# Optimization experiments

Hardware: AMD Instinct MI355X
Metric: run time of the kernel (lower is better)

The kernel has to match this reference:

```python
import jax, jax.numpy as jnp
import numpy as np

EMBED = 64
HEADS = 4
HEAD_DIM = EMBED // HEADS
N, T = 1024, 36


def setup_inputs() -> dict:
    key = jax.random.key(0)
    ks = jax.random.split(key, 8)
    scale = 1.0 / np.sqrt(HEAD_DIM)
    return {
        "values": jax.random.normal(ks[0], (N, T, EMBED), dtype=jnp.float32),
        "keys": jax.random.normal(ks[1], (N, T, EMBED), dtype=jnp.float32),
        "query": jax.random.normal(ks[2], (N, T, EMBED), dtype=jnp.float32),
        "Wv": jax.random.normal(ks[3], (HEAD_DIM, HEAD_DIM), dtype=jnp.float32) * scale,
        "Wk": jax.random.normal(ks[4], (HEAD_DIM, HEAD_DIM), dtype=jnp.float32) * scale,
        "Wq": jax.random.normal(ks[5], (HEAD_DIM, HEAD_DIM), dtype=jnp.float32) * scale,
        "Wo": jax.random.normal(ks[6], (EMBED, EMBED), dtype=jnp.float32) * (1.0 / np.sqrt(EMBED)),
        "bo": jax.random.normal(ks[7], (EMBED,), dtype=jnp.float32) * 0.01,
    }


def reference(values, keys, query, Wv, Wk, Wq, Wo, bo):
    n, t, c = query.shape
    h, d = HEADS, HEAD_DIM
    v = values.reshape(n, t, h, d)
    k = keys.reshape(n, t, h, d)
    q = query.reshape(n, t, h, d)
    # nn.Linear(head_dim, head_dim, bias=False): x @ W.T
    v = jnp.einsum('nthd,ed->nthe', v, Wv)
    k = jnp.einsum('nthd,ed->nthe', k, Wk)
    q = jnp.einsum('nthd,ed->nthe', q, Wq)
    # attention over the node dim: energy [N_q, N_k, T, H]
    energy = jnp.einsum('qthd,kthd->qkth', q, k)
    attention = jax.nn.softmax(energy / jnp.sqrt(jnp.float32(c)), axis=1)
    out = jnp.einsum('qkth,kthd->qthd', attention, v).reshape(n, t, h * d)
    return out @ Wo.T + bo
```

## Files before the change

### kernel.cpp

```cpp
#include <hip/hip_runtime.h>
#include <math.h>

#define N_NODES 1024
#define T_STEPS 36
#define KTILE   128
#define VTSTR   136
#define WOS     72
#define OBS2    72
#define YSTR6   17

typedef __bf16  bf16x8 __attribute__((ext_vector_type(8)));
typedef float   f32x4  __attribute__((ext_vector_type(4)));

#define MFMA_BF16 __builtin_amdgcn_mfma_f32_16x16x32_bf16
#define PERM_HI 0x07060302u
#define PERM_LO 0x05040100u

__device__ __forceinline__ unsigned short bf16_rne(float f) {
    unsigned int u = __float_as_uint(f);
    u += 0x7FFFu + ((u >> 16) & 1u);
    return (unsigned short)(u >> 16);
}
__device__ __forceinline__ float bf16_tof(unsigned short h) {
    return __uint_as_float(((unsigned int)h) << 16);
}

__global__ __launch_bounds__(128) void proj6_kernel(
    const float* __restrict__ vin, const float* __restrict__ kin, const float* __restrict__ qin,
    const float* __restrict__ Wv, const float* __restrict__ Wk, const float* __restrict__ Wq,
    unsigned short* __restrict__ qhi, unsigned short* __restrict__ qlo,
    unsigned short* __restrict__ khi, unsigned short* __restrict__ klo,
    unsigned short* __restrict__ vthi, unsigned short* __restrict__ vtlo)
{
    __shared__ float sW[256];
    __shared__ unsigned int ys[128 * YSTR6];

    const int tid = threadIdx.x;
    const int mat = blockIdx.y;
    const int nt  = blockIdx.x & 15;
    const int tt  = blockIdx.x >> 4;
    const int n0  = nt * 64, t0 = tt * 2;

    const float* in = (mat == 0) ? vin : (mat == 1) ? kin : qin;
    const float* W  = (mat == 0) ? Wv  : (mat == 1) ? Wk  : Wq;
    sW[tid] = W[tid]; sW[tid + 128] = W[tid + 128];
    __syncthreads();

    const int nl = tid >> 1, tl = tid & 1;
    const int n = n0 + nl, tcur = t0 + tl;
    const size_t ib = ((size_t)n * T_STEPS + tcur) * 64;
    const float scale = (mat == 2) ? 0.18033688011112042f : 1.0f;

    if (mat != 0) {
        unsigned short* ohi = (mat == 1) ? khi : qhi;
        unsigned short* olo = (mat == 1) ? klo : qlo;
        #pragma unroll
        for (int hd = 0; hd < 4; ++hd) {
            float xr[16];
            #pragma unroll
            for (int i = 0; i < 4; ++i) {
                float4 f = *(const float4*)(in + ib + hd*16 + 4*i);
                xr[4*i] = f.x; xr[4*i+1] = f.y; xr[4*i+2] = f.z; xr[4*i+3] = f.w;
            }
            union { unsigned short u[16]; uint4 v[2]; } hb, lb;
            #pragma unroll
            for (int e = 0; e < 16; ++e) {
                float4 w0 = *(const float4*)&sW[e*16+0],  w1 = *(const float4*)&sW[e*16+4];
                float4 w2 = *(const float4*)&sW[e*16+8],  w3 = *(const float4*)&sW[e*16+12];
                float a = xr[0]*w0.x;
                a = fmaf(xr[1],w0.y,a);  a = fmaf(xr[2],w0.z,a);  a = fmaf(xr[3],w0.w,a);
                a = fmaf(xr[4],w1.x,a);  a = fmaf(xr[5],w1.y,a);  a = fmaf(xr[6],w1.z,a);  a = fmaf(xr[7],w1.w,a);
                a = fmaf(xr[8],w2.x,a);  a = fmaf(xr[9],w2.y,a);  a = fmaf(xr[10],w2.z,a); a = fmaf(xr[11],w2.w,a);
                a = fmaf(xr[12],w3.x,a); a = fmaf(xr[13],w3.y,a); a = fmaf(xr[14],w3.z,a); a = fmaf(xr[15],w3.w,a);
                a *= scale;
                unsigned short hh = bf16_rne(a);
                hb.u[e] = hh; lb.u[e] = bf16_rne(a - bf16_tof(hh));
            }
            const int th = tcur * 4 + hd;
            const size_t off = ((size_t)th * N_NODES + n) * 16;
            *(uint4*)(ohi + off)     = hb.v[0];
            *(uint4*)(ohi + off + 8) = hb.v[1];
            *(uint4*)(olo + off)     = lb.v[0];
            *(uint4*)(olo + off + 8) = lb.v[1];
        }
    } else {
        #pragma unroll
        for (int hd = 0; hd < 4; ++hd) {
            {
                float xr[16];
                #pragma unroll
                for (int i = 0; i < 4; ++i) {
                    float4 f = *(const float4*)(in + ib + hd*16 + 4*i);
                    xr[4*i] = f.x; xr[4*i+1] = f.y; xr[4*i+2] = f.z; xr[4*i+3] = f.w;
                }
                unsigned int* yrow = &ys[tid * YSTR6];
                #pragma unroll
                for (int e = 0; e < 16; ++e) {
                    float4 w0 = *(const float4*)&sW[e*16+0],  w1 = *(const float4*)&sW[e*16+4];
                    float4 w2 = *(const float4*)&sW[e*16+8],  w3 = *(const float4*)&sW[e*16+12];
                    float a = xr[0]*w0.x;
                    a = fmaf(xr[1],w0.y,a);  a = fmaf(xr[2],w0.z,a);  a = fmaf(xr[3],w0.w,a);
                    a = fmaf(xr[4],w1.x,a);  a = fmaf(xr[5],w1.y,a);  a = fmaf(xr[6],w1.z,a);  a = fmaf(xr[7],w1.w,a);
                    a = fmaf(xr[8],w2.x,a);  a = fmaf(xr[9],w2.y,a);  a = fmaf(xr[10],w2.z,a); a = fmaf(xr[11],w2.w,a);
                    a = fmaf(xr[12],w3.x,a); a = fmaf(xr[13],w3.y,a); a = fmaf(xr[14],w3.z,a); a = fmaf(xr[15],w3.w,a);
                    unsigned short hh = bf16_rne(a);
                    unsigned short ll = bf16_rne(a - bf16_tof(hh));
                    yrow[e] = ((unsigned int)hh << 16) | ll;
                }
            }
            __syncthreads();
            {
                const int e = tid >> 3, ng = tid & 7;
                #pragma unroll
                for (int tl2 = 0; tl2 < 2; ++tl2) {
                    unsigned int u[8];
                    #pragma unroll
                    for (int j = 0; j < 8; ++j)
                        u[j] = ys[((ng*8 + j)*2 + tl2) * YSTR6 + e];
                    uint4 hi4, lo4;
                    hi4.x = __builtin_amdgcn_perm(u[1], u[0], PERM_HI);
                    hi4.y = __builtin_amdgcn_perm(u[3], u[2], PERM_HI);
                    hi4.z = __builtin_amdgcn_perm(u[5], u[4], PERM_HI);
                    hi4.w = __builtin_amdgcn_perm(u[7], u[6], PERM_HI);
                    lo4.x = __builtin_amdgcn_perm(u[1], u[0], PERM_LO);
                    lo4.y = __builtin_amdgcn_perm(u[3], u[2], PERM_LO);
                    lo4.z = __builtin_amdgcn_perm(u[5], u[4], PERM_LO);
                    lo4.w = __builtin_amdgcn_perm(u[7], u[6], PERM_LO);
                    const int th = (t0 + tl2) * 4 + hd;
                    const size_t off = ((size_t)th * 16 + e) * N_NODES + n0 + ng * 8;
                    *(uint4*)(vthi + off) = hi4;
                    *(uint4*)(vtlo + off) = lo4;
                }
            }
            if (hd < 3) __syncthreads();
        }
    }
}

__global__ __launch_bounds__(128, 5) void attn_mfma5_kernel(
    const unsigned short* __restrict__ qhi, const unsigned short* __restrict__ qlo,
    const unsigned short* __restrict__ khi, const unsigned short* __restrict__ klo,
    const unsigned short* __restrict__ vthi, const unsigned short* __restrict__ vtlo,
    unsigned short* __restrict__ obh, unsigned short* __restrict__ obl)
{
    __shared__ unsigned short vthi_s[16 * VTSTR];
    __shared__ unsigned short vtlo_s[16 * VTSTR];

    const int tid  = threadIdx.x;
    const int wave = tid >> 6, lane = tid & 63;
    const int m = lane & 15, quad = lane >> 4;

    const int bid = blockIdx.x;
    const int th  = bid % 144;
    const int qb  = bid / 144;
    const int t   = th >> 2, hd = th & 3;
    const int q0  = qb * 64;
    const size_t base_th = (size_t)th * N_NODES;

    const bf16x8 bzero = {};
    bf16x8 b1q[2], b2q[2];
    #pragma unroll
    for (int g = 0; g < 2; ++g) {
        const int qrow = q0 + wave * 32 + g * 16 + m;
        b1q[g] = *(const bf16x8*)(qhi + (base_th + qrow) * 16 + (quad & 1) * 8);
        b2q[g] = (quad < 2)
            ? *(const bf16x8*)(qlo + (base_th + qrow) * 16 + (quad & 1) * 8) : bzero;
    }

    union { unsigned short su[8]; bf16x8 v; } onesu;
    #pragma unroll
    for (int i = 0; i < 8; ++i) onesu.su[i] = 0x3F80;
    const bf16x8 bones = onesu.v;

    f32x4 og[2]   = {{0.f,0.f,0.f,0.f},{0.f,0.f,0.f,0.f}};
    f32x4 lacc[2] = {{0.f,0.f,0.f,0.f},{0.f,0.f,0.f,0.f}};

    const unsigned short* kfrag = ((quad < 2) ? khi : klo)
        + (base_th + m) * 16 + (quad & 1) * 8;

    const int vd = (tid >> 2) & 15, vpart = tid & 3;
    const unsigned short* vsrc0 = (wave ? vtlo : vthi)
        + ((size_t)th * 16 + vd) * N_NODES + vpart * 32;
    unsigned short* vdst = (wave ? vtlo_s : vthi_s) + vd * VTSTR + vpart * 32;

    uint4 pf0, pf1, pf2, pf3;
    { const uint4* s = (const uint4*)vsrc0; pf0 = s[0]; pf1 = s[1]; pf2 = s[2]; pf3 = s[3]; }

    for (int kt = 0; kt < N_NODES; kt += KTILE) {
        __syncthreads();
        *(uint2*)&vdst[0]  = make_uint2(pf0.x, pf0.y);
        *(uint2*)&vdst[8]  = make_uint2(pf0.z, pf0.w);
        *(uint2*)&vdst[16] = make_uint2(pf1.x, pf1.y);
        *(uint2*)&vdst[24] = make_uint2(pf1.z, pf1.w);
        *(uint2*)&vdst[4]  = make_uint2(pf2.x, pf2.y);
        *(uint2*)&vdst[12] = make_uint2(pf2.z, pf2.w);
        *(uint2*)&vdst[20] = make_uint2(pf3.x, pf3.y);
        *(uint2*)&vdst[28] = make_uint2(pf3.z, pf3.w);
        __syncthreads();
        if (kt + KTILE < N_NODES) {
            const uint4* s = (const uint4*)(vsrc0 + kt + KTILE);
            pf0 = s[0]; pf1 = s[1]; pf2 = s[2]; pf3 = s[3];
        }

        #pragma unroll
        for (int c = 0; c < 4; ++c) {
            bf16x8 a0 = *(const bf16x8*)(kfrag + (size_t)(kt + (2*c    )*16) * 16);
            bf16x8 a1 = *(const bf16x8*)(kfrag + (size_t)(kt + (2*c + 1)*16) * 16);
            bf16x8 vh = *(const bf16x8*)&vthi_s[m * VTSTR + quad * 8 + c * 32];
            bf16x8 vl = *(const bf16x8*)&vtlo_s[m * VTSTR + quad * 8 + c * 32];
            #pragma unroll
            for (int g = 0; g < 2; ++g) {
                f32x4 s0 = MFMA_BF16(a0, b1q[g], (f32x4){0.f,0.f,0.f,0.f}, 0, 0, 0);
                s0 = MFMA_BF16(a0, b2q[g], s0, 0, 0, 0);
                f32x4 s1 = MFMA_BF16(a1, b1q[g], (f32x4){0.f,0.f,0.f,0.f}, 0, 0, 0);
                s1 = MFMA_BF16(a1, b2q[g], s1, 0, 0, 0);
                union { __bf16 b[8]; bf16x8 v; } ap;
                ap.b[0] = (__bf16)__builtin_amdgcn_exp2f(s0[0]);
                ap.b[1] = (__bf16)__builtin_amdgcn_exp2f(s0[1]);
                ap.b[2] = (__bf16)__builtin_amdgcn_exp2f(s0[2]);
                ap.b[3] = (__bf16)__builtin_amdgcn_exp2f(s0[3]);
                ap.b[4] = (__bf16)__builtin_amdgcn_exp2f(s1[0]);
                ap.b[5] = (__bf16)__builtin_amdgcn_exp2f(s1[1]);
                ap.b[6] = (__bf16)__builtin_amdgcn_exp2f(s1[2]);
                ap.b[7] = (__bf16)__builtin_amdgcn_exp2f(s1[3]);
                lacc[g] = MFMA_BF16(ap.v, bones, lacc[g], 0, 0, 0);
                og[g]   = MFMA_BF16(ap.v, vh, og[g], 0, 0, 0);
                og[g]   = MFMA_BF16(ap.v, vl, og[g], 0, 0, 0);
            }
        }
    }

    #pragma unroll
    for (int g = 0; g < 2; ++g) {
        #pragma unroll
        for (int r = 0; r < 4; ++r) {
            const float val = og[g][r] * __builtin_amdgcn_rcpf(lacc[g][r]);
            const int row = q0 + wave * 32 + g * 16 + quad * 4 + r;
            const size_t off = ((size_t)row * T_STEPS + t) * 64 + hd * 16 + m;
            unsigned short hh = bf16_rne(val);
            obh[off] = hh;
            obl[off] = bf16_rne(val - bf16_tof(hh));
        }
    }
}

__global__ __launch_bounds__(256) void outproj_mfma_kernel(
    const unsigned short* __restrict__ obh, const unsigned short* __restrict__ obl,
    const float* __restrict__ Wo, const float* __restrict__ bo,
    float* __restrict__ out)
{
    __shared__ unsigned short woh[64 * WOS], wol[64 * WOS];
    __shared__ unsigned short oth[64 * OBS2], otl[64 * OBS2];
    __shared__ float sb[64];
    const int tid = threadIdx.x;

    #pragma unroll
    for (int i = 0; i < 16; ++i) {
        int idx = tid + 256 * i;
        int r = idx >> 6, c = idx & 63;
        float w = Wo[idx];
        unsigned short hh = bf16_rne(w);
        woh[r * WOS + c] = hh;
        wol[r * WOS + c] = bf16_rne(w - bf16_tof(hh));
    }
    if (tid < 64) sb[tid] = bo[tid];

    const size_t p0 = (size_t)blockIdx.x * 64;
    #pragma unroll
    for (int i = 0; i < 2; ++i) {
        int idx = tid + 256 * i;
        int r = idx >> 3, c = (idx & 7) * 8;
        *(uint4*)&oth[r * OBS2 + c] = *(const uint4*)(obh + (p0 + r) * 64 + c);
        *(uint4*)&otl[r * OBS2 + c] = *(const uint4*)(obl + (p0 + r) * 64 + c);
    }
    __syncthreads();

    const int wave = tid >> 6, lane = tid & 63;
    const int m = lane & 15, quad = lane >> 4;
    const int r0 = wave * 16;

    bf16x8 ah[2], al[2];
    #pragma unroll
    for (int kh = 0; kh < 2; ++kh) {
        ah[kh] = *(const bf16x8*)&oth[(r0 + m) * OBS2 + kh * 32 + quad * 8];
        al[kh] = *(const bf16x8*)&otl[(r0 + m) * OBS2 + kh * 32 + quad * 8];
    }

    f32x4 acc[4] = {{0,0,0,0},{0,0,0,0},{0,0,0,0},{0,0,0,0}};
    #pragma unroll
    for (int jt = 0; jt < 4; ++jt) {
        #pragma unroll
        for (int kh = 0; kh < 2; ++kh) {
            bf16x8 bh = *(const bf16x8*)&woh[(jt * 16 + m) * WOS + kh * 32 + quad * 8];
            bf16x8 bl = *(const bf16x8*)&wol[(jt * 16 + m) * WOS + kh * 32 + quad * 8];
            acc[jt] = MFMA_BF16(ah[kh], bh, acc[jt], 0, 0, 0);
            acc[jt] = MFMA_BF16(al[kh], bh, acc[jt], 0, 0, 0);
            acc[jt] = MFMA_BF16(ah[kh], bl, acc[jt], 0, 0, 0);
        }
    }

    #pragma unroll
    for (int jt = 0; jt < 4; ++jt) {
        const float b = sb[jt * 16 + m];
        #pragma unroll
        for (int r = 0; r < 4; ++r)
            out[(p0 + r0 + quad * 4 + r) * 64 + jt * 16 + m] = acc[jt][r] + b;
    }
}

extern "C" void kernel_launch(void* const* d_in, const int* in_sizes, int n_in,
                              void* d_out, int out_size, void* d_ws, size_t ws_size,
                              hipStream_t stream)
{
    (void)in_sizes; (void)n_in; (void)out_size; (void)ws_size;
    const float* values = (const float*)d_in[0];
    const float* keys   = (const float*)d_in[1];
    const float* query  = (const float*)d_in[2];
    const float* Wv     = (const float*)d_in[3];
    const float* Wk     = (const float*)d_in[4];
    const float* Wq     = (const float*)d_in[5];
    const float* Wo     = (const float*)d_in[6];
    const float* bo     = (const float*)d_in[7];

    const size_t TOT = (size_t)144 * N_NODES * 16;
    unsigned short* ws16 = (unsigned short*)d_ws;
    unsigned short* qhi  = ws16;
    unsigned short* qlo  = ws16 + 1*TOT;
    unsigned short* khi  = ws16 + 2*TOT;
    unsigned short* klo  = ws16 + 3*TOT;
    unsigned short* vthi = ws16 + 4*TOT;
    unsigned short* vtlo = ws16 + 5*TOT;
    unsigned short* obh  = ws16 + 6*TOT;
    unsigned short* obl  = ws16 + 7*TOT;

    proj6_kernel<<<dim3(288, 3), 128, 0, stream>>>(values, keys, query, Wv, Wk, Wq,
                                                   qhi, qlo, khi, klo, vthi, vtlo);
    attn_mfma5_kernel<<<dim3(16 * 144), 128, 0, stream>>>(qhi, qlo, khi, klo, vthi, vtlo,
                                                          obh, obl);
    outproj_mfma_kernel<<<dim3(576), 256, 0, stream>>>(obh, obl, Wo, bo, (float*)d_out);
}
```

Measured before the change: 138.7 us.

## Split projection rows across thread pairs and batch V transpose with one barrier

The projection kernel now covers 32 nodes per block instead of 64 and doubles the grid. Each thread handles half a row (two heads) and loads all 32 inputs up front. For the V path, all four heads are staged into a wider shared buffer first, then transposed after a single barrier instead of one barrier per head. Each thread now writes either the hi or the lo plane. The goal is more blocks, more memory parallelism and fewer syncs, at the cost of more registers and more shared memory per block.

```diff
diff --git a/kernel.cpp b/kernel.cpp
--- a/kernel.cpp
+++ b/kernel.cpp
@@ -7,7 +7,7 @@
 #define VTSTR   136
 #define WOS     72
 #define OBS2    72
-#define YSTR6   17
+#define YSTR7   65
 
 typedef __bf16  bf16x8 __attribute__((ext_vector_type(8)));
 typedef float   f32x4  __attribute__((ext_vector_type(4)));
@@ -25,7 +25,7 @@
     return __uint_as_float(((unsigned int)h) << 16);
 }
 
-__global__ __launch_bounds__(128) void proj6_kernel(
+__global__ __launch_bounds__(128, 4) void proj7_kernel(
     const float* __restrict__ vin, const float* __restrict__ kin, const float* __restrict__ qin,
     const float* __restrict__ Wv, const float* __restrict__ Wk, const float* __restrict__ Wq,
     unsigned short* __restrict__ qhi, unsigned short* __restrict__ qlo,
@@ -33,35 +33,38 @@
     unsigned short* __restrict__ vthi, unsigned short* __restrict__ vtlo)
 {
     __shared__ float sW[256];
-    __shared__ unsigned int ys[128 * YSTR6];
+    __shared__ unsigned int ys[64 * YSTR7];
 
     const int tid = threadIdx.x;
     const int mat = blockIdx.y;
-    const int nt  = blockIdx.x & 15;
-    const int tt  = blockIdx.x >> 4;
-    const int n0  = nt * 64, t0 = tt * 2;
+    const int nt  = blockIdx.x & 31;
+    const int tt  = blockIdx.x >> 5;
+    const int n0  = nt * 32, t0 = tt * 2;
 
     const float* in = (mat == 0) ? vin : (mat == 1) ? kin : qin;
     const float* W  = (mat == 0) ? Wv  : (mat == 1) ? Wk  : Wq;
     sW[tid] = W[tid]; sW[tid + 128] = W[tid + 128];
     __syncthreads();
 
-    const int nl = tid >> 1, tl = tid & 1;
+    const int rl = tid >> 1, hp = tid & 1;
+    const int nl = rl >> 1, tl = rl & 1;
     const int n = n0 + nl, tcur = t0 + tl;
-    const size_t ib = ((size_t)n * T_STEPS + tcur) * 64;
+    const size_t ib = ((size_t)n * T_STEPS + tcur) * 64 + hp * 32;
     const float scale = (mat == 2) ? 0.18033688011112042f : 1.0f;
+
+    float x[32];
+    #pragma unroll
+    for (int i = 0; i < 8; ++i) {
+        float4 f = *(const float4*)(in + ib + 4*i);
+        x[4*i] = f.x; x[4*i+1] = f.y; x[4*i+2] = f.z; x[4*i+3] = f.w;
+    }
 
     if (mat != 0) {
         unsigned short* ohi = (mat == 1) ? khi : qhi;
         unsigned short* olo = (mat == 1) ? klo : qlo;
         #pragma unroll
-        for (int hd = 0; hd < 4; ++hd) {
-            float xr[16];
-            #pragma unroll
-            for (int i = 0; i < 4; ++i) {
-                float4 f = *(const float4*)(in + ib + hd*16 + 4*i);
-                xr[4*i] = f.x; xr[4*i+1] = f.y; xr[4*i+2] = f.z; xr[4*i+3] = f.w;
-            }
+        for (int hd2 = 0; hd2 < 2; ++hd2) {
+            const float* xr = &x[hd2 * 16];
             union { unsigned short u[16]; uint4 v[2]; } hb, lb;
             #pragma unroll
             for (int e = 0; e < 16; ++e) {
@@ -76,7 +79,7 @@
                 unsigned short hh = bf16_rne(a);
                 hb.u[e] = hh; lb.u[e] = bf16_rne(a - bf16_tof(hh));
             }
-            const int th = tcur * 4 + hd;
+            const int th = tcur * 4 + hp * 2 + hd2;
             const size_t off = ((size_t)th * N_NODES + n) * 16;
             *(uint4*)(ohi + off)     = hb.v[0];
             *(uint4*)(ohi + off + 8) = hb.v[1];
@@ -85,54 +88,43 @@
         }
     } else {
         #pragma unroll
-        for (int hd = 0; hd < 4; ++hd) {
-            {
-                float xr[16];
-                #pragma unroll
-                for (int i = 0; i < 4; ++i) {
-                    float4 f = *(const float4*)(in + ib + hd*16 + 4*i);
-                    xr[4*i] = f.x; xr[4*i+1] = f.y; xr[4*i+2] = f.z; xr[4*i+3] = f.w;
-                }
-                unsigned int* yrow = &ys[tid * YSTR6];
-                #pragma unroll
-                for (int e = 0; e < 16; ++e) {
-                    float4 w0 = *(const float4*)&sW[e*16+0],  w1 = *(const float4*)&sW[e*16+4];
-                    float4 w2 = *(const float4*)&sW[e*16+8],  w3 = *(const float4*)&sW[e*16+12];
-                    float a = xr[0]*w0.x;
-                    a = fmaf(xr[1],w0.y,a);  a = fmaf(xr[2],w0.z,a);  a = fmaf(xr[3],w0.w,a);
-                    a = fmaf(xr[4],w1.x,a);  a = fmaf(xr[5],w1.y,a);  a = fmaf(xr[6],w1.z,a);  a = fmaf(xr[7],w1.w,a);
-                    a = fmaf(xr[8],w2.x,a);  a = fmaf(xr[9],w2.y,a);  a = fmaf(xr[10],w2.z,a); a = fmaf(xr[11],w2.w,a);
-                    a = fmaf(xr[12],w3.x,a); a = fmaf(xr[13],w3.y,a); a = fmaf(xr[14],w3.z,a); a = fmaf(xr[15],w3.w,a);
-                    unsigned short hh = bf16_rne(a);
-                    unsigned short ll = bf16_rne(a - bf16_tof(hh));
-                    yrow[e] = ((unsigned int)hh << 16) | ll;
-                }
+        for (int hd2 = 0; hd2 < 2; ++hd2) {
+            const float* xr = &x[hd2 * 16];
+            unsigned int* yrow = &ys[rl * YSTR7 + (hp * 2 + hd2) * 16];
+            #pragma unroll
+            for (int e = 0; e < 16; ++e) {
+                float4 w0 = *(const float4*)&sW[e*16+0],  w1 = *(const float4*)&sW[e*16+4];
+                float4 w2 = *(const float4*)&sW[e*16+8],  w3 = *(const float4*)&sW[e*16+12];
+                float a = xr[0]*w0.x;
+                a = fmaf(xr[1],w0.y,a);  a = fmaf(xr[2],w0.z,a);  a = fmaf(xr[3],w0.w,a);
+                a = fmaf(xr[4],w1.x,a);  a = fmaf(xr[5],w1.y,a);  a = fmaf(xr[6],w1.z,a);  a = fmaf(xr[7],w1.w,a);
+                a = fmaf(xr[8],w2.x,a);  a = fmaf(xr[9],w2.y,a);  a = fmaf(xr[10],w2.z,a); a = fmaf(xr[11],w2.w,a);
+                a = fmaf(xr[12],w3.x,a); a = fmaf(xr[13],w3.y,a); a = fmaf(xr[14],w3.z,a); a = fmaf(xr[15],w3.w,a);
+                unsigned short hh = bf16_rne(a);
+                unsigned short ll = bf16_rne(a - bf16_tof(hh));
+                yrow[e] = ((unsigned int)hh << 16) | ll;
             }
-            __syncthreads();
-            {
-                const int e = tid >> 3, ng = tid & 7;
-                #pragma unroll
-                for (int tl2 = 0; tl2 < 2; ++tl2) {
-                    unsigned int u[8];
-                    #pragma unroll
-                    for (int j = 0; j < 8; ++j)
-                        u[j] = ys[((ng*8 + j)*2 + tl2) * YSTR6 + e];
-                    uint4 hi4, lo4;
-                    hi4.x = __builtin_amdgcn_perm(u[1], u[0], PERM_HI);
-                    hi4.y = __builtin_amdgcn_perm(u[3], u[2], PERM_HI);
-                    hi4.z = __builtin_amdgcn_perm(u[5], u[4], PERM_HI);
-                    hi4.w = __builtin_amdgcn_perm(u[7], u[6], PERM_HI);
-                    lo4.x = __builtin_amdgcn_perm(u[1], u[0], PERM_LO);
-                    lo4.y = __builtin_amdgcn_perm(u[3], u[2], PERM_LO);
-                    lo4.z = __builtin_amdgcn_perm(u[5], u[4], PERM_LO);
-                    lo4.w = __builtin_amdgcn_perm(u[7], u[6], PERM_LO);
-                    const int th = (t0 + tl2) * 4 + hd;
-                    const size_t off = ((size_t)th * 16 + e) * N_NODES + n0 + ng * 8;
-                    *(uint4*)(vthi + off) = hi4;
-                    *(uint4*)(vtlo + off) = lo4;
-                }
-            }
-            if (hd < 3) __syncthreads();
+        }
+        __syncthreads();
+        const int e = tid >> 3, q8 = tid & 7;
+        const int sel = q8 >> 2, oct = q8 & 3;
+        #pragma unroll
+        for (int p = 0; p < 8; ++p) {
+            const int tl2 = p & 1, hd = p >> 1;
+            unsigned int u[8];
+            #pragma unroll
+            for (int j = 0; j < 8; ++j)
+                u[j] = ys[((oct*8 + j)*2 + tl2) * YSTR7 + hd*16 + e];
+            const unsigned int pm = sel ? PERM_LO : PERM_HI;
+            uint4 o4;
+            o4.x = __builtin_amdgcn_perm(u[1], u[0], pm);
+            o4.y = __builtin_amdgcn_perm(u[3], u[2], pm);
+            o4.z = __builtin_amdgcn_perm(u[5], u[4], pm);
+            o4.w = __builtin_amdgcn_perm(u[7], u[6], pm);
+            const int th = (t0 + tl2) * 4 + hd;
+            unsigned short* dst = (sel ? vtlo : vthi)
+                + ((size_t)th * 16 + e) * N_NODES + n0 + oct * 8;
+            *(uint4*)dst = o4;
         }
     }
 }
@@ -333,7 +325,7 @@
     unsigned short* obh  = ws16 + 6*TOT;
     unsigned short* obl  = ws16 + 7*TOT;
 
-    proj6_kernel<<<dim3(288, 3), 128, 0, stream>>>(values, keys, query, Wv, Wk, Wq,
+    proj7_kernel<<<dim3(576, 3), 128, 0, stream>>>(values, keys, query, Wv, Wk, Wq,
                                                    qhi, qlo, khi, klo, vthi, vtlo);
     attn_mfma5_kernel<<<dim3(16 * 144), 128, 0, stream>>>(qhi, qlo, khi, klo, vthi, vtlo,
                                                           obh, obl);
```

After: 194.7 us. +40.3%, slower.
